# Performance work log

Measured on AMD Instinct MI355X. Metric: run time of the kernel, lower is better.

## Reference

```python
import jax, jax.numpy as jnp
from jax import lax
import numpy as np

B, L, D, KSIZE = 16, 1024, 256, 16


def setup_inputs() -> dict:
    key = jax.random.key(0)
    ks = jax.random.split(key, 5)
    s = 1.0 / np.sqrt(D)  # torch RNN init scale
    return {
        "x": jax.random.normal(ks[0], (B, L, D), dtype=jnp.float32),
        "W_ih": jax.random.uniform(ks[1], (3 * D, D), jnp.float32, -s, s),
        "W_hh": jax.random.uniform(ks[2], (3 * D, D), jnp.float32, -s, s),
        "b_ih": jax.random.uniform(ks[3], (3 * D,), jnp.float32, -s, s),
        "b_hh": jax.random.uniform(ks[4], (3 * D,), jnp.float32, -s, s),
        "ksize": KSIZE,
    }


def _windows(x, ksize):
    # Left-pad with ksize-1 zero rows, then take overlapping windows of length ksize.
    b, l, d = x.shape
    xpad = jnp.concatenate([jnp.zeros((b, ksize - 1, d), x.dtype), x], axis=1)
    idx = jnp.arange(l)[:, None] + jnp.arange(ksize)[None, :]  # (l, ksize)
    return xpad[:, idx]  # (b, l, ksize, d)


def _gru_last(x_seq, W_ih, W_hh, b_ih, b_hh):
    # x_seq: (N, ksize, d) -> final hidden state (N, d). Torch GRU cell math.
    n_batch, _, d = x_seq.shape
    gi_all = jnp.einsum('nkd,gd->nkg', x_seq, W_ih) + b_ih  # precompute input gates

    def step(h, gi):
        gh = h @ W_hh.T + b_hh
        i_r, i_z, i_n = jnp.split(gi, 3, axis=-1)
        h_r, h_z, h_n = jnp.split(gh, 3, axis=-1)
        r = jax.nn.sigmoid(i_r + h_r)
        z = jax.nn.sigmoid(i_z + h_z)
        n = jnp.tanh(i_n + r * h_n)
        h_new = (1.0 - z) * n + z * h
        return h_new, None

    h0 = jnp.zeros((n_batch, d), x_seq.dtype)
    hT, _ = lax.scan(step, h0, jnp.swapaxes(gi_all, 0, 1))
    return hT


def reference(x, W_ih, W_hh, b_ih, b_hh, ksize):
    b, l, d = x.shape
    win = _windows(x, ksize).reshape(b * l, ksize, d)  # (b*l, ksize, d)
    h = _gru_last(win, W_ih, W_hh, b_ih, b_hh)         # (b*l, d)
    return h.reshape(b, l, d)
```

## Files before the change

### kernel.cpp

```cpp
#include <hip/hip_runtime.h>

#define B_SZ 16
#define L_SZ 1024
#define D_SZ 256
#define KW   16

typedef float f32x4 __attribute__((ext_vector_type(4)));
typedef short bf16x8 __attribute__((ext_vector_type(8)));
typedef unsigned int u32x4 __attribute__((ext_vector_type(4)));
typedef unsigned int u32x2 __attribute__((ext_vector_type(2)));

__device__ __forceinline__ float bf2f(unsigned short u) {
    union { unsigned int i; float f; } v; v.i = ((unsigned int)u) << 16; return v.f;
}
__device__ __forceinline__ unsigned short f2bf(float f) {
    union { float f; unsigned int i; } v; v.f = f;
    unsigned int r = v.i + 0x7fffu + ((v.i >> 16) & 1u);
    return (unsigned short)(r >> 16);
}
__device__ __forceinline__ float fast_sigmoid(float x) {
    float e = __builtin_amdgcn_exp2f(-1.44269504f * x);
    return __builtin_amdgcn_rcpf(1.0f + e);
}
__device__ __forceinline__ float fast_tanh(float x) {
    float e = __builtin_amdgcn_exp2f(-2.88539008f * x);
    return (1.0f - e) * __builtin_amdgcn_rcpf(1.0f + e);
}
__device__ __forceinline__ f32x4 zero4() { f32x4 v; v[0]=0.f; v[1]=0.f; v[2]=0.f; v[3]=0.f; return v; }

__global__ void prep_kernel(const float* __restrict__ wih,
                            const float* __restrict__ whh,
                            unsigned short* __restrict__ wpkih,
                            unsigned short* __restrict__ wpkhh) {
    const int NW = 768 * 256;
    for (int i = blockIdx.x * blockDim.x + threadIdx.x; i < 2 * NW;
         i += gridDim.x * blockDim.x) {
        const float* W = (i < NW) ? wih : whh;
        unsigned short* dst = (i < NW) ? wpkih : wpkhh;
        int t = (i < NW) ? i : (i - NW);
        int j = t & 7;
        int q = t >> 3;
        int colg = q & 15; q >>= 4;
        int kg = q & 3;    q >>= 2;
        int ks = q & 7;    q >>= 3;
        int g = q % 3;
        int wid = q / 3;
        int src = (g * 256 + wid * 16 + colg) * 256 + ks * 32 + kg * 8 + j;
        dst[t] = f2bf(W[src]);
    }
}

#define GI_PITCH 1536
#define XW_BASE  121344
#define LDS_BYTES (121344 + 80*512)

__global__ __launch_bounds__(1024, 1) void rnn_v4(
    const float* __restrict__ x,
    const unsigned short* __restrict__ wpkih,
    const unsigned short* __restrict__ wpkhh,
    const float* __restrict__ bih,
    const float* __restrict__ bhh,
    float* __restrict__ out) {
    __shared__ u32x4 ldsv[LDS_BYTES / 16];
    char* lds = (char*)ldsv;
    char* gi = lds;
    char* xw = lds + XW_BASE;
    char* hb = lds + XW_BASE;

    const int tid = threadIdx.x;
    const int wid = tid >> 6, lane = tid & 63;
    const int b = blockIdx.x >> 4;
    const int l0 = (blockIdx.x & 15) << 6;
    const int colg = lane & 15;
    const int kg = (lane >> 4) & 3;
    const int dcol = wid * 16 + colg;

    for (int c = tid; c < 5120; c += 1024) {
        int row = c >> 6;
        int f0 = (c & 63) * 4;
        int gl = l0 - (KW - 1) + row;
        u32x2 pk;
        if (gl >= 0 && gl < L_SZ) {
            f32x4 v = *(const f32x4*)(x + ((size_t)(b * L_SZ + gl)) * 256 + f0);
            pk[0] = (unsigned int)f2bf(v[0]) | ((unsigned int)f2bf(v[1]) << 16);
            pk[1] = (unsigned int)f2bf(v[2]) | ((unsigned int)f2bf(v[3]) << 16);
        } else {
            pk[0] = 0u; pk[1] = 0u;
        }
        *(u32x2*)(xw + row * 512 + ((f0 * 2) ^ ((row & 7) << 4))) = pk;
    }
    __syncthreads();

    {
        const unsigned short* wb = wpkih + (size_t)wid * 12288;
        const float bi0 = bih[dcol];
        const float bi1 = bih[256 + dcol];
        const float bi2 = bih[512 + dcol];
#pragma unroll 1
        for (int tile = 0; tile < 5; tile++) {
            f32x4 a0 = zero4(), a1 = zero4(), a2 = zero4();
#pragma unroll
            for (int ks = 0; ks < 8; ks++) {
                bf16x8 w0 = *(const bf16x8*)(wb + (0 * 8 + ks) * 512 + lane * 8);
                bf16x8 w1 = *(const bf16x8*)(wb + (1 * 8 + ks) * 512 + lane * 8);
                bf16x8 w2 = *(const bf16x8*)(wb + (2 * 8 + ks) * 512 + lane * 8);
                int row = tile * 16 + colg;
                bf16x8 a = *(const bf16x8*)(xw + row * 512 +
                                            ((ks * 64 + kg * 16) ^ ((row & 7) << 4)));
                a0 = __builtin_amdgcn_mfma_f32_16x16x32_bf16(a, w0, a0, 0, 0, 0);
                a1 = __builtin_amdgcn_mfma_f32_16x16x32_bf16(a, w1, a1, 0, 0, 0);
                a2 = __builtin_amdgcn_mfma_f32_16x16x32_bf16(a, w2, a2, 0, 0, 0);
            }
#pragma unroll
            for (int rr = 0; rr < 4; rr++) {
                int row = tile * 16 + kg * 4 + rr;
                if (row < 79) {
                    int sw = (row & 7) << 4;
                    char* gr = gi + row * GI_PITCH;
                    *(unsigned short*)(gr + ((dcol * 2) ^ sw)) = f2bf(a0[rr] + bi0);
                    *(unsigned short*)(gr + ((512 + dcol * 2) ^ sw)) = f2bf(a1[rr] + bi1);
                    *(unsigned short*)(gr + ((1024 + dcol * 2) ^ sw)) = f2bf(a2[rr] + bi2);
                }
            }
        }
    }
    __syncthreads();

    const unsigned short* wb = wpkhh + (size_t)wid * 12288;
    const float bz0 = bhh[dcol];
    const float bz1 = bhh[256 + dcol];
    const float bhn = bhh[512 + dcol];

    f32x4 hst[4];
#pragma unroll
    for (int mt = 0; mt < 4; mt++) hst[mt] = zero4();

#pragma unroll 1
    for (int k = 0; k < KW; k++) {
        f32x4 arz0[4], arz1[4], ahn[4];
#pragma unroll
        for (int mt = 0; mt < 4; mt++) {
            arz0[mt] = zero4(); arz1[mt] = zero4(); ahn[mt] = zero4();
        }

        if (k > 0) {
#pragma unroll
            for (int ks = 0; ks < 8; ks++) {
                bf16x8 w0 = *(const bf16x8*)(wb + (0 * 8 + ks) * 512 + lane * 8);
                bf16x8 w1 = *(const bf16x8*)(wb + (1 * 8 + ks) * 512 + lane * 8);
                bf16x8 w2 = *(const bf16x8*)(wb + (2 * 8 + ks) * 512 + lane * 8);
                const int kcol = ks * 64 + kg * 16;
#pragma unroll
                for (int mt = 0; mt < 4; mt++) {
                    int row = mt * 16 + colg;
                    bf16x8 a = *(const bf16x8*)(hb + row * 512 +
                                                (kcol ^ ((row & 7) << 4)));
                    arz0[mt] = __builtin_amdgcn_mfma_f32_16x16x32_bf16(a, w0, arz0[mt], 0, 0, 0);
                    arz1[mt] = __builtin_amdgcn_mfma_f32_16x16x32_bf16(a, w1, arz1[mt], 0, 0, 0);
                    ahn[mt]  = __builtin_amdgcn_mfma_f32_16x16x32_bf16(a, w2, ahn[mt], 0, 0, 0);
                }
            }
        }
        __syncthreads();

#pragma unroll
        for (int mt = 0; mt < 4; mt++) {
#pragma unroll
            for (int rr = 0; rr < 4; rr++) {
                int row = mt * 16 + kg * 4 + rr;
                int xrow = k + row;
                int sw = (xrow & 7) << 4;
                const char* gr = gi + xrow * GI_PITCH;
                float ir  = bf2f(*(const unsigned short*)(gr + ((dcol * 2) ^ sw)));
                float iz  = bf2f(*(const unsigned short*)(gr + ((512 + dcol * 2) ^ sw)));
                float in_ = bf2f(*(const unsigned short*)(gr + ((1024 + dcol * 2) ^ sw)));
                float r = fast_sigmoid(ir + arz0[mt][rr] + bz0);
                float z = fast_sigmoid(iz + arz1[mt][rr] + bz1);
                float n = fast_tanh(in_ + r * (ahn[mt][rr] + bhn));
                float h = hst[mt][rr];
                float hnew = n + z * (h - n);
                hst[mt][rr] = hnew;
                *(unsigned short*)(hb + row * 512 +
                                   ((dcol * 2) ^ ((row & 7) << 4))) = f2bf(hnew);
            }
        }
        __syncthreads();
    }

#pragma unroll
    for (int mt = 0; mt < 4; mt++) {
#pragma unroll
        for (int rr = 0; rr < 4; rr++) {
            int row = mt * 16 + kg * 4 + rr;
            out[((size_t)(b * L_SZ + l0 + row)) * D_SZ + dcol] = hst[mt][rr];
        }
    }
}

extern "C" void kernel_launch(void* const* d_in, const int* in_sizes, int n_in,
                              void* d_out, int out_size, void* d_ws, size_t ws_size,
                              hipStream_t stream) {
    const float* x   = (const float*)d_in[0];
    const float* wih = (const float*)d_in[1];
    const float* whh = (const float*)d_in[2];
    const float* bih = (const float*)d_in[3];
    const float* bhh = (const float*)d_in[4];
    float* out = (float*)d_out;

    char* ws = (char*)d_ws;
    unsigned short* wpkih = (unsigned short*)(ws);
    unsigned short* wpkhh = (unsigned short*)(ws + 393216);

    prep_kernel<<<512, 256, 0, stream>>>(wih, whh, wpkih, wpkhh);
    rnn_v4<<<256, 1024, 0, stream>>>(x, wpkih, wpkhh, bih, bhh, out);
}
```

Measured before the change: 331.5 us.

## Halve block size so each wave computes two column slices of the GRU

The GRU kernel now launches 512 threads per block instead of 1024. Each wave loops over two 128-column halves for both the input-gate precompute and the recurrent step. The previous hidden state is re-read from LDS as bf16 instead of being kept in fp32 registers. New bf16 values are staged in packed registers and written to LDS between two barriers, and the final step writes the output directly. This trades thread-level parallelism for more work per wave. It also keeps the recurrence state at lower precision.

```diff
diff --git a/kernel.cpp b/kernel.cpp
--- a/kernel.cpp
+++ b/kernel.cpp
@@ -44,8 +44,8 @@
         int kg = q & 3;    q >>= 2;
         int ks = q & 7;    q >>= 3;
         int g = q % 3;
-        int wid = q / 3;
-        int src = (g * 256 + wid * 16 + colg) * 256 + ks * 32 + kg * 8 + j;
+        int s = q / 3;
+        int src = (g * 256 + s * 16 + colg) * 256 + ks * 32 + kg * 8 + j;
         dst[t] = f2bf(W[src]);
     }
 }
@@ -54,7 +54,7 @@
 #define XW_BASE  121344
 #define LDS_BYTES (121344 + 80*512)
 
-__global__ __launch_bounds__(1024, 1) void rnn_v4(
+__global__ __launch_bounds__(512, 2) void rnn_v7(
     const float* __restrict__ x,
     const unsigned short* __restrict__ wpkih,
     const unsigned short* __restrict__ wpkhh,
@@ -73,9 +73,8 @@
     const int l0 = (blockIdx.x & 15) << 6;
     const int colg = lane & 15;
     const int kg = (lane >> 4) & 3;
-    const int dcol = wid * 16 + colg;
-
-    for (int c = tid; c < 5120; c += 1024) {
+
+    for (int c = tid; c < 5120; c += 512) {
         int row = c >> 6;
         int f0 = (c & 63) * 4;
         int gl = l0 - (KW - 1) + row;
@@ -91,11 +90,13 @@
     }
     __syncthreads();
 
-    {
-        const unsigned short* wb = wpkih + (size_t)wid * 12288;
-        const float bi0 = bih[dcol];
-        const float bi1 = bih[256 + dcol];
-        const float bi2 = bih[512 + dcol];
+#pragma unroll 1
+    for (int hp = 0; hp < 2; hp++) {
+        const unsigned short* wb = wpkih + (size_t)(hp * 8 + wid) * 12288;
+        const int dc = hp * 128 + wid * 16 + colg;
+        const float bi0 = bih[dc];
+        const float bi1 = bih[256 + dc];
+        const float bi2 = bih[512 + dc];
 #pragma unroll 1
         for (int tile = 0; tile < 5; tile++) {
             f32x4 a0 = zero4(), a1 = zero4(), a2 = zero4();
@@ -117,82 +118,102 @@
                 if (row < 79) {
                     int sw = (row & 7) << 4;
                     char* gr = gi + row * GI_PITCH;
-                    *(unsigned short*)(gr + ((dcol * 2) ^ sw)) = f2bf(a0[rr] + bi0);
-                    *(unsigned short*)(gr + ((512 + dcol * 2) ^ sw)) = f2bf(a1[rr] + bi1);
-                    *(unsigned short*)(gr + ((1024 + dcol * 2) ^ sw)) = f2bf(a2[rr] + bi2);
+                    *(unsigned short*)(gr + ((dc * 2) ^ sw)) = f2bf(a0[rr] + bi0);
+                    *(unsigned short*)(gr + ((512 + dc * 2) ^ sw)) = f2bf(a1[rr] + bi1);
+                    *(unsigned short*)(gr + ((1024 + dc * 2) ^ sw)) = f2bf(a2[rr] + bi2);
                 }
             }
         }
     }
     __syncthreads();
-
-    const unsigned short* wb = wpkhh + (size_t)wid * 12288;
-    const float bz0 = bhh[dcol];
-    const float bz1 = bhh[256 + dcol];
-    const float bhn = bhh[512 + dcol];
-
-    f32x4 hst[4];
-#pragma unroll
-    for (int mt = 0; mt < 4; mt++) hst[mt] = zero4();
 
 #pragma unroll 1
     for (int k = 0; k < KW; k++) {
-        f32x4 arz0[4], arz1[4], ahn[4];
-#pragma unroll
-        for (int mt = 0; mt < 4; mt++) {
-            arz0[mt] = zero4(); arz1[mt] = zero4(); ahn[mt] = zero4();
-        }
-
-        if (k > 0) {
-#pragma unroll
-            for (int ks = 0; ks < 8; ks++) {
-                bf16x8 w0 = *(const bf16x8*)(wb + (0 * 8 + ks) * 512 + lane * 8);
-                bf16x8 w1 = *(const bf16x8*)(wb + (1 * 8 + ks) * 512 + lane * 8);
-                bf16x8 w2 = *(const bf16x8*)(wb + (2 * 8 + ks) * 512 + lane * 8);
-                const int kcol = ks * 64 + kg * 16;
+        unsigned int hnewpk[2][8];
+#pragma unroll
+        for (int hp = 0; hp < 2; hp++) {
+            const int dc = hp * 128 + wid * 16 + colg;
+            const float bz0 = bhh[dc];
+            const float bz1 = bhh[256 + dc];
+            const float bhn = bhh[512 + dc];
+
+            f32x4 ar[4], az[4], an_[4];
+#pragma unroll
+            for (int mt = 0; mt < 4; mt++) {
+                ar[mt] = zero4(); az[mt] = zero4(); an_[mt] = zero4();
+            }
+
+            if (k > 0) {
+                const unsigned short* wb = wpkhh + (size_t)(hp * 8 + wid) * 12288;
+#pragma unroll
+                for (int ks = 0; ks < 8; ks++) {
+                    bf16x8 w0 = *(const bf16x8*)(wb + (0 * 8 + ks) * 512 + lane * 8);
+                    bf16x8 w1 = *(const bf16x8*)(wb + (1 * 8 + ks) * 512 + lane * 8);
+                    bf16x8 w2 = *(const bf16x8*)(wb + (2 * 8 + ks) * 512 + lane * 8);
+                    const int kcol = ks * 64 + kg * 16;
+#pragma unroll
+                    for (int mt = 0; mt < 4; mt++) {
+                        int row = mt * 16 + colg;
+                        bf16x8 a = *(const bf16x8*)(hb + row * 512 +
+                                                    (kcol ^ ((row & 7) << 4)));
+                        ar[mt]  = __builtin_amdgcn_mfma_f32_16x16x32_bf16(a, w0, ar[mt], 0, 0, 0);
+                        az[mt]  = __builtin_amdgcn_mfma_f32_16x16x32_bf16(a, w1, az[mt], 0, 0, 0);
+                        an_[mt] = __builtin_amdgcn_mfma_f32_16x16x32_bf16(a, w2, an_[mt], 0, 0, 0);
+                    }
+                }
+            }
+
+#pragma unroll
+            for (int mt = 0; mt < 4; mt++) {
+#pragma unroll
+                for (int rr = 0; rr < 4; rr++) {
+                    int row = mt * 16 + kg * 4 + rr;
+                    int xrow = k + row;
+                    int sw = (xrow & 7) << 4;
+                    const char* gr = gi + xrow * GI_PITCH;
+                    float ir  = bf2f(*(const unsigned short*)(gr + ((dc * 2) ^ sw)));
+                    float iz  = bf2f(*(const unsigned short*)(gr + ((512 + dc * 2) ^ sw)));
+                    float in_ = bf2f(*(const unsigned short*)(gr + ((1024 + dc * 2) ^ sw)));
+                    float hold = (k > 0)
+                        ? bf2f(*(const unsigned short*)(hb + row * 512 +
+                                                        ((dc * 2) ^ ((row & 7) << 4))))
+                        : 0.0f;
+                    float r = fast_sigmoid(ir + ar[mt][rr] + bz0);
+                    float z = fast_sigmoid(iz + az[mt][rr] + bz1);
+                    float n = fast_tanh(in_ + r * (an_[mt][rr] + bhn));
+                    float hnew = n + z * (hold - n);
+                    if (k == KW - 1) {
+                        out[((size_t)(b * L_SZ + l0 + row)) * D_SZ + dc] = hnew;
+                    } else {
+                        int e = mt * 4 + rr;
+                        unsigned int bfv = f2bf(hnew);
+                        if (e & 1) hnewpk[hp][e >> 1] |= bfv << 16;
+                        else       hnewpk[hp][e >> 1]  = bfv;
+                    }
+                }
+            }
+        }
+
+        if (k < KW - 1) {
+            __syncthreads();
+#pragma unroll
+            for (int hp = 0; hp < 2; hp++) {
+                const int dc = hp * 128 + wid * 16 + colg;
 #pragma unroll
                 for (int mt = 0; mt < 4; mt++) {
-                    int row = mt * 16 + colg;
-                    bf16x8 a = *(const bf16x8*)(hb + row * 512 +
-                                                (kcol ^ ((row & 7) << 4)));
-                    arz0[mt] = __builtin_amdgcn_mfma_f32_16x16x32_bf16(a, w0, arz0[mt], 0, 0, 0);
-                    arz1[mt] = __builtin_amdgcn_mfma_f32_16x16x32_bf16(a, w1, arz1[mt], 0, 0, 0);
-                    ahn[mt]  = __builtin_amdgcn_mfma_f32_16x16x32_bf16(a, w2, ahn[mt], 0, 0, 0);
-                }
-            }
-        }
-        __syncthreads();
-
-#pragma unroll
-        for (int mt = 0; mt < 4; mt++) {
-#pragma unroll
-            for (int rr = 0; rr < 4; rr++) {
-                int row = mt * 16 + kg * 4 + rr;
-                int xrow = k + row;
-                int sw = (xrow & 7) << 4;
-                const char* gr = gi + xrow * GI_PITCH;
-                float ir  = bf2f(*(const unsigned short*)(gr + ((dcol * 2) ^ sw)));
-                float iz  = bf2f(*(const unsigned short*)(gr + ((512 + dcol * 2) ^ sw)));
-                float in_ = bf2f(*(const unsigned short*)(gr + ((1024 + dcol * 2) ^ sw)));
-                float r = fast_sigmoid(ir + arz0[mt][rr] + bz0);
-                float z = fast_sigmoid(iz + arz1[mt][rr] + bz1);
-                float n = fast_tanh(in_ + r * (ahn[mt][rr] + bhn));
-                float h = hst[mt][rr];
-                float hnew = n + z * (h - n);
-                hst[mt][rr] = hnew;
-                *(unsigned short*)(hb + row * 512 +
-                                   ((dcol * 2) ^ ((row & 7) << 4))) = f2bf(hnew);
-            }
-        }
-        __syncthreads();
-    }
-
-#pragma unroll
-    for (int mt = 0; mt < 4; mt++) {
-#pragma unroll
-        for (int rr = 0; rr < 4; rr++) {
-            int row = mt * 16 + kg * 4 + rr;
-            out[((size_t)(b * L_SZ + l0 + row)) * D_SZ + dcol] = hst[mt][rr];
+#pragma unroll
+                    for (int rr = 0; rr < 4; rr++) {
+                        int row = mt * 16 + kg * 4 + rr;
+                        int e = mt * 4 + rr;
+                        unsigned int w = hnewpk[hp][e >> 1];
+                        unsigned short hv = (e & 1) ? (unsigned short)(w >> 16)
+                                                    : (unsigned short)(w & 0xffff);
+                        *(unsigned short*)(hb + row * 512 +
+                                           ((dc * 2) ^ ((row & 7) << 4))) = hv;
+                    }
+                }
+            }
+            __syncthreads();
         }
     }
 }
@@ -212,5 +233,5 @@
     unsigned short* wpkhh = (unsigned short*)(ws + 393216);
 
     prep_kernel<<<512, 256, 0, stream>>>(wih, whh, wpkih, wpkhh);
-    rnn_v4<<<256, 1024, 0, stream>>>(x, wpkih, wpkhh, bih, bhh, out);
-}
+    rnn_v7<<<256, 512, 0, stream>>>(x, wpkih, wpkhh, bih, bhh, out);
+}
```

Result: slower. 373.3 us (+12.6%).
